# Performance work log

Measured on AMD Instinct MI355X. Metric: run time of the kernel, lower is better.

Reference implementation:

```python
import jax, jax.numpy as jnp
import numpy as np
from jax import lax

# Kernel / geometry constants matching init_kwargs
KZ, KX, KY = 9, 15, 15          # PSF support
STRIDE = (1, 1, 1)              # scale = (zscale, xscale, yscale)
Z_PAD = (KZ - 1 + 1) // 2       # 4
X_PAD = (KX - 1 + 1) // 2       # 7
Y_PAD = (KY - 1 + 1) // 2       # 7


def _dist(n):
    # |idx - n//2|, matching _distance_from_center
    return jnp.abs(jnp.arange(n, dtype=jnp.float32) - n // 2)


def gen_psf(bet_xy, bet_z, alpha):
    b = bet_xy.shape[0]
    zd = _dist(KZ)                                  # [KZ]
    xd = _dist(KX)
    yd = _dist(KY)
    # gen_distance_plane: dp[i, j] = xd[j]^2 + yd[i]^2  (shape [KY, KX])
    dp = yd[:, None] ** 2 + xd[None, :] ** 2
    # gen_2dnorm: [b, KY, KX]
    bxy = bet_xy[:, None, None]
    lat = jnp.exp(-dp[None] / (2.0 * bxy ** 2)) / (2.0 * jnp.pi * bxy ** 2)
    # gen_1dnorm: [b, KZ]
    bz = bet_z[:, None]
    ax = jnp.exp(-(zd[None] ** 2) / (2.0 * bz ** 2)) / (jnp.sqrt(2.0 * jnp.pi) * bz)
    # psf = exp(log(lateral) + log(axial)) == lateral * axial  -> [b, 1, KZ, KY, KX]
    psf = lat[:, None, None, :, :] * ax[:, None, :, None, None]
    # double_exp mode
    psf = 1.0 - jnp.exp(-alpha[:, None, None, None, None] * psf)
    return psf / jnp.sum(psf)


def reference(x, bet_xy, bet_z, alpha):
    # x: [B, 1, Z, X, Y]; original computes dense conv3d giving [B, B, ...] and
    # keeps only the diagonal _x[b, b]. That is mathematically a per-sample
    # (grouped) convolution, implemented here without the O(B) redundancy.
    psf = gen_psf(bet_xy, bet_z, alpha)             # [B, 1, KZ, KY, KX]
    B = x.shape[0]
    xin = jnp.transpose(x, (1, 0, 2, 3, 4))         # [1, B, Z, X, Y]
    out = lax.conv_general_dilated(
        xin, psf,
        window_strides=STRIDE,
        padding=[(Z_PAD, Z_PAD), (X_PAD, X_PAD), (Y_PAD, Y_PAD)],
        dimension_numbers=("NCDHW", "OIDHW", "NCDHW"),
        feature_group_count=B,
    )                                               # [1, B, Z', X', Y']
    return jnp.transpose(out, (1, 0, 2, 3, 4))      # [B, 1, Z', X', Y']


def setup_inputs() -> dict:
    key = jax.random.key(0)
    k1, k2, k3, k4 = jax.random.split(key, 4)
    B = 4
    x = jax.random.normal(k1, (B, 1, 32, 192, 192), dtype=jnp.float32)
    bet_xy = 1.0 + 2.0 * jax.random.uniform(k2, (B,), dtype=jnp.float32)   # in [1, 3)
    bet_z = 1.0 + 2.0 * jax.random.uniform(k3, (B,), dtype=jnp.float32)    # in [1, 3)
    alpha = 1.0 + 9.0 * jax.random.uniform(k4, (B,), dtype=jnp.float32)    # in [1, 10)
    return {"x": x, "bet_xy": bet_xy, "bet_z": bet_z, "alpha": alpha}
```

## Files before the change

kernel.cpp:

```cpp
#include <hip/hip_runtime.h>
#include <math.h>

#define B_ 4
#define D_ 32
#define H_ 192
#define W_ 192
#define HW_ (H_ * W_)

#define NT 5

#define TW 48
#define TH 12
#define NTHR 256
#define ZCHUNK 16
#define NPLANES (ZCHUNK + 8)

#define XT_H 26
#define XT_COLS 62
#define XT_W 80
#define XT_CELLS (XT_H * XT_COLS)
#define NSEC 7

#define R_S 48
#define R_H 26

#define NTAPS (B_ * 9 * 15 * 15)

__device__ inline float4 f4fma(float c, float4 a, float4 d) {
    d.x = fmaf(c, a.x, d.x); d.y = fmaf(c, a.y, d.y);
    d.z = fmaf(c, a.z, d.z); d.w = fmaf(c, a.w, d.w);
    return d;
}
__device__ inline float4 f4add(float4 a, float4 b) {
    a.x += b.x; a.y += b.y; a.z += b.z; a.w += b.w; return a;
}

__global__ __launch_bounds__(NTHR)
void conv_kernel(const float* __restrict__ x,
                 const float* __restrict__ bet_xy,
                 const float* __restrict__ bet_z,
                 const float* __restrict__ alpha,
                 float* __restrict__ out) {
    __shared__ __align__(16) float xt[XT_H * XT_W];
    __shared__ __align__(16) float Rb[NT][R_H * R_S];
    __shared__ float ct[NT][16];
    __shared__ float red[NTHR];

    const int t  = threadIdx.x;
    const int w0 = blockIdx.x * TW;
    const int h0 = blockIdx.y * TH;
    const int bz = blockIdx.z;
    const int b  = bz & 3;
    const int z0 = (bz >> 2) * ZCHUNK;
    const float INV = 0.3989422804014327f;

    float local = 0.f;
#pragma unroll
    for (int s = 0; s < 32; ++s) {
        int idx = t + s * NTHR;
        if (idx < NTAPS) {
            int bb = idx / 2025;
            int r  = idx % 2025;
            int dz = r / 225;
            int r2 = r % 225;
            int dh = r2 / 15;
            int dw = r2 % 15;
            float bxy = bet_xy[bb], bzv = bet_z[bb], al = alpha[bb];
            float zd = (float)(dz - 4), hd = (float)(dh - 7), wd = (float)(dw - 7);
            float az = expf(-zd * zd / (2.f * bzv * bzv)) * (INV / bzv);
            float gh = expf(-hd * hd / (2.f * bxy * bxy)) * (INV / bxy);
            float gw = expf(-wd * wd / (2.f * bxy * bxy)) * (INV / bxy);
            local += 1.f - expf(-al * az * gh * gw);
        }
    }
    red[t] = local;
    __syncthreads();
    for (int s = 128; s > 0; s >>= 1) {
        if (t < s) red[t] += red[t + s];
        __syncthreads();
    }
    const float S = red[0];

    if (t < NT * 13) {
        int n = t / 13;
        int k = t % 13;
        float bxy = bet_xy[b], bzv = bet_z[b], al = alpha[b];
        if (k < 8) {
            float d = (float)k;
            float g = expf(-d * d / (2.f * bxy * bxy)) * (INV / bxy);
            float p = g;
            for (int q = 0; q < n; ++q) p *= g;
            ct[n][k] = p;
        } else {
            float d = (float)(k - 8);
            float az = expf(-d * d / (2.f * bzv * bzv)) * (INV / bzv);
            float base = al * az;
            float p = base;
            for (int q = 0; q < n; ++q) p *= base;
            const float facs[NT] = {1.f, 2.f, 6.f, 24.f, 120.f};
            float sign = (n & 1) ? -1.f : 1.f;
            ct[n][k] = sign * p / (facs[n] * S);
        }
    }

    const float* xb = x + (size_t)b * (D_ * HW_);
    int goff[NSEC], loff[NSEC];
#pragma unroll
    for (int k = 0; k < NSEC; ++k) {
        int i = t + k * NTHR;
        int r = i / XT_COLS, c = i - r * XT_COLS;
        int gh = h0 + r - 7, gw = w0 + c - 7;
        bool ok = (i < XT_CELLS) && gh >= 0 && gh < H_ && gw >= 0 && gw < W_;
        goff[k] = ok ? (gh * W_ + gw) : -1;
        loff[k] = (i < XT_CELLS) ? (r * XT_W + c) : (XT_H * XT_W - 1);
    }
    {
        int zi0 = z0 - 4;
        if (zi0 >= 0) {
#pragma unroll
            for (int k = 0; k < NSEC; ++k) {
                float v = 0.f;
                if (goff[k] >= 0) v = xb[(size_t)zi0 * HW_ + goff[k]];
                xt[loff[k]] = v;
            }
        }
    }

    const int i0r = t / 12,  i0c = t - 12 * i0r;
    const int i1  = t + NTHR;
    const int i1r = i1 / 12, i1c = i1 - 12 * i1r;
    const bool sec1 = (i1 < XT_H * 12);
    const int wb0 = i0r * XT_W + 4 * i0c, rw0 = i0r * R_S + 4 * i0c;
    const int wb1 = i1r * XT_W + 4 * i1c, rw1 = i1r * R_S + 4 * i1c;
    const bool hact = (t < TH * 12);
    const int ro = t / 12, cgh = t - 12 * ro;
    const int hb = ro * R_S + 4 * cgh;

    float4 acc[9];
#pragma unroll
    for (int k = 0; k < 9; ++k) acc[k] = make_float4(0.f, 0.f, 0.f, 0.f);

    for (int p = 0; p < NPLANES; ++p) {
        const int zi = z0 - 4 + p;
        const bool valid = (zi >= 0) && (zi < D_);
        __syncthreads();

        const int zn = zi + 1;
        const bool more = (p < NPLANES - 1) && (zn >= 0) && (zn < D_);
        float pv[NSEC];
        if (more) {
            const float* xp = xb + (size_t)zn * HW_;
#pragma unroll
            for (int k = 0; k < NSEC; ++k) pv[k] = (goff[k] >= 0) ? xp[goff[k]] : 0.f;
        }

        if (valid) {
#pragma unroll
            for (int sec = 0; sec < 2; ++sec) {
                if (sec == 1 && !sec1) break;
                const int wb = sec ? wb1 : wb0;
                const int rw = sec ? rw1 : rw0;
                float win[20];
                {
                    const float4* p4 = (const float4*)&xt[wb];
#pragma unroll
                    for (int q = 0; q < 5; ++q) {
                        float4 a = p4[q];
                        win[4 * q] = a.x; win[4 * q + 1] = a.y;
                        win[4 * q + 2] = a.z; win[4 * q + 3] = a.w;
                    }
                }
                float cj[4], sp[4][7];
#pragma unroll
                for (int j = 0; j < 4; ++j) {
                    cj[j] = win[j + 7];
#pragma unroll
                    for (int k = 1; k <= 7; ++k) sp[j][k - 1] = win[j + 7 - k] + win[j + 7 + k];
                }
#pragma unroll
                for (int n = 0; n < NT; ++n) {
                    const float* g = ct[n];
                    float4 a;
                    a.x = g[0] * cj[0]; a.y = g[0] * cj[1];
                    a.z = g[0] * cj[2]; a.w = g[0] * cj[3];
#pragma unroll
                    for (int k = 1; k <= 7; ++k) {
                        float c = g[k];
                        a.x = fmaf(c, sp[0][k - 1], a.x);
                        a.y = fmaf(c, sp[1][k - 1], a.y);
                        a.z = fmaf(c, sp[2][k - 1], a.z);
                        a.w = fmaf(c, sp[3][k - 1], a.w);
                    }
                    *(float4*)&Rb[n][rw] = a;
                }
            }
        }
        __syncthreads();

        if (valid && hact) {
#pragma unroll
            for (int n = 0; n < NT; ++n) {
                const float* Rr = Rb[n];
                const float* g  = ct[n];
                float4 rv[15];
#pragma unroll
                for (int dh = 0; dh < 15; ++dh)
                    rv[dh] = *(const float4*)&Rr[hb + dh * R_S];
                float4 q;
                q.x = g[0] * rv[7].x; q.y = g[0] * rv[7].y;
                q.z = g[0] * rv[7].z; q.w = g[0] * rv[7].w;
#pragma unroll
                for (int k = 1; k <= 7; ++k)
                    q = f4fma(g[k], f4add(rv[7 - k], rv[7 + k]), q);
                acc[4] = f4fma(g[8], q, acc[4]);
#pragma unroll
                for (int j = 1; j <= 4; ++j) {
                    float cz = g[8 + j];
                    acc[4 + j] = f4fma(cz, q, acc[4 + j]);
                    acc[4 - j] = f4fma(cz, q, acc[4 - j]);
                }
            }
        }

        if (hact) {
            if (p >= 8) {
                int z = zi - 4;
                size_t o = ((size_t)(b * D_ + z) * H_ + (h0 + ro)) * W_ + (w0 + 4 * cgh);
                *(float4*)&out[o] = acc[0];
            }
#pragma unroll
            for (int k = 0; k < 8; ++k) acc[k] = acc[k + 1];
            acc[8] = make_float4(0.f, 0.f, 0.f, 0.f);
        }

        if (more) {
#pragma unroll
            for (int k = 0; k < NSEC; ++k) xt[loff[k]] = pv[k];
        }
    }
}

extern "C" void kernel_launch(void* const* d_in, const int* in_sizes, int n_in,
                              void* d_out, int out_size, void* d_ws, size_t ws_size,
                              hipStream_t stream) {
    const float* x      = (const float*)d_in[0];
    const float* bet_xy = (const float*)d_in[1];
    const float* bet_z  = (const float*)d_in[2];
    const float* alpha  = (const float*)d_in[3];
    float* out = (float*)d_out;

    hipLaunchKernelGGL(conv_kernel, dim3(W_ / TW, H_ / TH, B_ * (D_ / ZCHUNK)),
                       dim3(NTHR), 0, stream, x, bet_xy, bet_z, alpha, out);
}
```

Baseline: 158.2 us.

## Double-buffer input and row buffers to pipeline W and H passes across planes

The input tile and the W-pass result buffers are double-buffered, so the H/Z pass for plane p-1 runs in the same iteration as the W pass for plane p. This removes one block barrier per plane. The per-sample coefficients are moved from shared memory into uniform registers via readfirstlane. The W-pass work split is rebalanced so the second section uses threads 200-255 rather than leaving the first section's remainder uneven, and the xt row stride is reduced. The cost is more shared memory, which may lower occupancy, plus more register pressure from the coefficient arrays.

```diff
diff --git a/kernel.cpp b/kernel.cpp
--- a/kernel.cpp
+++ b/kernel.cpp
@@ -13,16 +13,19 @@
 #define TH 12
 #define NTHR 256
 #define ZCHUNK 16
-#define NPLANES (ZCHUNK + 8)
+#define NP (ZCHUNK + 8)
 
 #define XT_H 26
 #define XT_COLS 62
-#define XT_W 80
+#define XT_W 72
 #define XT_CELLS (XT_H * XT_COLS)
 #define NSEC 7
 
 #define R_S 48
 #define R_H 26
+
+#define XT_SZ (XT_H * XT_W)
+#define SMEM_WORDS (2 * XT_SZ + 2 * NT * R_H * R_S)
 
 #define NTAPS (B_ * 9 * 15 * 15)
 
@@ -33,6 +36,9 @@
 }
 __device__ inline float4 f4add(float4 a, float4 b) {
     a.x += b.x; a.y += b.y; a.z += b.z; a.w += b.w; return a;
+}
+__device__ inline float rfl(float x) {
+    return __int_as_float(__builtin_amdgcn_readfirstlane(__float_as_int(x)));
 }
 
 __global__ __launch_bounds__(NTHR)
@@ -41,10 +47,11 @@
                  const float* __restrict__ bet_z,
                  const float* __restrict__ alpha,
                  float* __restrict__ out) {
-    __shared__ __align__(16) float xt[XT_H * XT_W];
-    __shared__ __align__(16) float Rb[NT][R_H * R_S];
-    __shared__ float ct[NT][16];
-    __shared__ float red[NTHR];
+    __shared__ __align__(16) float smem[SMEM_WORDS];
+    float* xtb = smem;
+    float* Rb  = smem + 2 * XT_SZ;
+    float* red = smem;
+    float* ct  = smem + 512;
 
     const int t  = threadIdx.x;
     const int w0 = blockIdx.x * TW;
@@ -80,6 +87,7 @@
         __syncthreads();
     }
     const float S = red[0];
+    __syncthreads();
 
     if (t < NT * 13) {
         int n = t / 13;
@@ -90,7 +98,7 @@
             float g = expf(-d * d / (2.f * bxy * bxy)) * (INV / bxy);
             float p = g;
             for (int q = 0; q < n; ++q) p *= g;
-            ct[n][k] = p;
+            ct[n * 16 + k] = p;
         } else {
             float d = (float)(k - 8);
             float az = expf(-d * d / (2.f * bzv * bzv)) * (INV / bzv);
@@ -99,9 +107,20 @@
             for (int q = 0; q < n; ++q) p *= base;
             const float facs[NT] = {1.f, 2.f, 6.f, 24.f, 120.f};
             float sign = (n & 1) ? -1.f : 1.f;
-            ct[n][k] = sign * p / (facs[n] * S);
-        }
-    }
+            ct[n * 16 + k] = sign * p / (facs[n] * S);
+        }
+    }
+    __syncthreads();
+
+    float cg_[NT][8], cz_[NT][5];
+#pragma unroll
+    for (int n = 0; n < NT; ++n) {
+#pragma unroll
+        for (int k = 0; k < 8; ++k) cg_[n][k] = rfl(ct[n * 16 + k]);
+#pragma unroll
+        for (int k = 0; k < 5; ++k) cz_[n][k] = rfl(ct[n * 16 + 8 + k]);
+    }
+    __syncthreads();
 
     const float* xb = x + (size_t)b * (D_ * HW_);
     int goff[NSEC], loff[NSEC];
@@ -112,7 +131,7 @@
         int gh = h0 + r - 7, gw = w0 + c - 7;
         bool ok = (i < XT_CELLS) && gh >= 0 && gh < H_ && gw >= 0 && gw < W_;
         goff[k] = ok ? (gh * W_ + gw) : -1;
-        loff[k] = (i < XT_CELLS) ? (r * XT_W + c) : (XT_H * XT_W - 1);
+        loff[k] = (i < XT_CELLS) ? (r * XT_W + c) : (XT_SZ - 1);
     }
     {
         int zi0 = z0 - 4;
@@ -121,15 +140,15 @@
             for (int k = 0; k < NSEC; ++k) {
                 float v = 0.f;
                 if (goff[k] >= 0) v = xb[(size_t)zi0 * HW_ + goff[k]];
-                xt[loff[k]] = v;
+                xtb[loff[k]] = v;
             }
         }
     }
 
     const int i0r = t / 12,  i0c = t - 12 * i0r;
-    const int i1  = t + NTHR;
+    const int i1  = t + 56;
     const int i1r = i1 / 12, i1c = i1 - 12 * i1r;
-    const bool sec1 = (i1 < XT_H * 12);
+    const bool sec1 = (t >= 200);
     const int wb0 = i0r * XT_W + 4 * i0c, rw0 = i0r * R_S + 4 * i0c;
     const int wb1 = i1r * XT_W + 4 * i1c, rw1 = i1r * R_S + 4 * i1c;
     const bool hact = (t < TH * 12);
@@ -140,21 +159,25 @@
 #pragma unroll
     for (int k = 0; k < 9; ++k) acc[k] = make_float4(0.f, 0.f, 0.f, 0.f);
 
-    for (int p = 0; p < NPLANES; ++p) {
+#pragma unroll 1
+    for (int p = 0; p <= NP; ++p) {
+        __syncthreads();
+
         const int zi = z0 - 4 + p;
-        const bool valid = (zi >= 0) && (zi < D_);
-        __syncthreads();
-
-        const int zn = zi + 1;
-        const bool more = (p < NPLANES - 1) && (zn >= 0) && (zn < D_);
+        const bool do_w  = (p < NP) && (zi >= 0) && (zi < D_);
+        const int  zn    = zi + 1;
+        const bool pvalid = (p + 1 < NP) && (zn >= 0) && (zn < D_);
+
         float pv[NSEC];
-        if (more) {
+        if (pvalid) {
             const float* xp = xb + (size_t)zn * HW_;
 #pragma unroll
             for (int k = 0; k < NSEC; ++k) pv[k] = (goff[k] >= 0) ? xp[goff[k]] : 0.f;
         }
 
-        if (valid) {
+        if (do_w) {
+            const float* xt = xtb + (p & 1) * XT_SZ;
+            float* Rw = Rb + (p & 1) * (NT * R_H * R_S);
 #pragma unroll
             for (int sec = 0; sec < 2; ++sec) {
                 if (sec == 1 && !sec1) break;
@@ -179,63 +202,64 @@
                 }
 #pragma unroll
                 for (int n = 0; n < NT; ++n) {
-                    const float* g = ct[n];
                     float4 a;
-                    a.x = g[0] * cj[0]; a.y = g[0] * cj[1];
-                    a.z = g[0] * cj[2]; a.w = g[0] * cj[3];
+                    a.x = cg_[n][0] * cj[0]; a.y = cg_[n][0] * cj[1];
+                    a.z = cg_[n][0] * cj[2]; a.w = cg_[n][0] * cj[3];
 #pragma unroll
                     for (int k = 1; k <= 7; ++k) {
-                        float c = g[k];
+                        float c = cg_[n][k];
                         a.x = fmaf(c, sp[0][k - 1], a.x);
                         a.y = fmaf(c, sp[1][k - 1], a.y);
                         a.z = fmaf(c, sp[2][k - 1], a.z);
                         a.w = fmaf(c, sp[3][k - 1], a.w);
                     }
-                    *(float4*)&Rb[n][rw] = a;
+                    *(float4*)&Rw[n * (R_H * R_S) + rw] = a;
                 }
             }
         }
-        __syncthreads();
-
-        if (valid && hact) {
-#pragma unroll
-            for (int n = 0; n < NT; ++n) {
-                const float* Rr = Rb[n];
-                const float* g  = ct[n];
-                float4 rv[15];
-#pragma unroll
-                for (int dh = 0; dh < 15; ++dh)
-                    rv[dh] = *(const float4*)&Rr[hb + dh * R_S];
-                float4 q;
-                q.x = g[0] * rv[7].x; q.y = g[0] * rv[7].y;
-                q.z = g[0] * rv[7].z; q.w = g[0] * rv[7].w;
-#pragma unroll
-                for (int k = 1; k <= 7; ++k)
-                    q = f4fma(g[k], f4add(rv[7 - k], rv[7 + k]), q);
-                acc[4] = f4fma(g[8], q, acc[4]);
-#pragma unroll
-                for (int j = 1; j <= 4; ++j) {
-                    float cz = g[8 + j];
-                    acc[4 + j] = f4fma(cz, q, acc[4 + j]);
-                    acc[4 - j] = f4fma(cz, q, acc[4 - j]);
-                }
+
+        if (p >= 1) {
+            const int ziq = zi - 1;
+            if (hact) {
+                if (ziq >= 0 && ziq < D_) {
+                    const float* Rr = Rb + ((p - 1) & 1) * (NT * R_H * R_S);
+#pragma unroll
+                    for (int n = 0; n < NT; ++n) {
+                        const float* R1 = Rr + n * (R_H * R_S);
+                        float4 rv[15];
+#pragma unroll
+                        for (int dh = 0; dh < 15; ++dh)
+                            rv[dh] = *(const float4*)&R1[hb + dh * R_S];
+                        float4 q;
+                        q.x = cg_[n][0] * rv[7].x; q.y = cg_[n][0] * rv[7].y;
+                        q.z = cg_[n][0] * rv[7].z; q.w = cg_[n][0] * rv[7].w;
+#pragma unroll
+                        for (int k = 1; k <= 7; ++k)
+                            q = f4fma(cg_[n][k], f4add(rv[7 - k], rv[7 + k]), q);
+                        acc[4] = f4fma(cz_[n][0], q, acc[4]);
+#pragma unroll
+                        for (int j = 1; j <= 4; ++j) {
+                            float cz = cz_[n][j];
+                            acc[4 + j] = f4fma(cz, q, acc[4 + j]);
+                            acc[4 - j] = f4fma(cz, q, acc[4 - j]);
+                        }
+                    }
+                }
+                if (p - 1 >= 8) {
+                    int z = z0 + (p - 1 - 8);
+                    size_t o = ((size_t)(b * D_ + z) * H_ + (h0 + ro)) * W_ + (w0 + 4 * cgh);
+                    *(float4*)&out[o] = acc[0];
+                }
+#pragma unroll
+                for (int k = 0; k < 8; ++k) acc[k] = acc[k + 1];
+                acc[8] = make_float4(0.f, 0.f, 0.f, 0.f);
             }
         }
 
-        if (hact) {
-            if (p >= 8) {
-                int z = zi - 4;
-                size_t o = ((size_t)(b * D_ + z) * H_ + (h0 + ro)) * W_ + (w0 + 4 * cgh);
-                *(float4*)&out[o] = acc[0];
-            }
-#pragma unroll
-            for (int k = 0; k < 8; ++k) acc[k] = acc[k + 1];
-            acc[8] = make_float4(0.f, 0.f, 0.f, 0.f);
-        }
-
-        if (more) {
-#pragma unroll
-            for (int k = 0; k < NSEC; ++k) xt[loff[k]] = pv[k];
+        if (pvalid) {
+            float* xn = xtb + ((p + 1) & 1) * XT_SZ;
+#pragma unroll
+            for (int k = 0; k < NSEC; ++k) xn[loff[k]] = pv[k];
         }
     }
 }
```

Result: no change. 157.0 us (-0.8%).
